# Kernel optimization log

Hardware: AMD Instinct MI355X
Metric: run time of the kernel (lower is better)

Reference implementation:

```python
import jax, jax.numpy as jnp
import numpy as np


def setup_inputs() -> dict:
    key = jax.random.key(0)
    k1, k2 = jax.random.split(key)
    B, H, W, C = 16, 4, 900, 256
    input_1 = jax.random.normal(k1, (B, H, W, C), dtype=jnp.float32)
    input_2 = jax.random.normal(k2, (B, H, W, C), dtype=jnp.float32)
    return {"input_1": input_1, "input_2": input_2}


def reference(input_1, input_2):
    # Original op: circularly pad input_1 along W (shift by n_pad), frame into W
    # overlapping windows of length W, multiply by input_2 and sum over (H, W, C).
    # Equivalent math: out[b, s] = sum_w <x1[b, :, (s + w + n_pad) % W, :],
    #                                     x2[b, :, w, :]>  (inner product over H, C).
    # We compute the [B, W, W] Gram matrix with a GEMM, then reduce the circular
    # diagonal bands -- avoids materializing the W-times framed [B, H, W, W, C].
    B, H, W, C = input_1.shape
    n_pad = W // 2
    D = H * C
    a1 = jnp.transpose(input_1, (0, 2, 1, 3)).reshape(B, W, D)  # [B, W, H*C]
    a2 = jnp.transpose(input_2, (0, 2, 1, 3)).reshape(B, W, D)
    gram = jnp.einsum('bid,bjd->bij', a1, a2)  # gram[b, i, j] = <x1_i, x2_j>
    s = jnp.arange(W)[:, None]   # shift index
    w = jnp.arange(W)[None, :]   # window position
    idx = (s + w + n_pad) % W    # [W, W] circular gather indices
    out = jnp.sum(gram[:, idx, w], axis=-1)  # [B, W]
    return out
```

## Files before the change

kernel.cpp:

```cpp
#include <hip/hip_runtime.h>
#include <stdint.h>

typedef __attribute__((ext_vector_type(8))) short short8;
typedef __attribute__((ext_vector_type(8))) unsigned short ushort8;
typedef __attribute__((ext_vector_type(4))) float floatx4;

#define W_DIM 900
#define PADW  1024
#define DDIM  1024
#define NPAD  450
#define TM    256
#define TN    128
#define BK    64

__device__ __forceinline__ unsigned short f2bf(float f) {
  unsigned int u = __builtin_bit_cast(unsigned int, f);
  u += 0x7fffu + ((u >> 16) & 1u);
  return (unsigned short)(u >> 16);
}

__device__ __forceinline__ void async16(const void* g, void* l) {
  __builtin_amdgcn_global_load_lds(
      (const __attribute__((address_space(1))) void*)g,
      (__attribute__((address_space(3))) void*)l, 16, 0, 0);
}

__global__ void convert_kernel(const float* __restrict__ in1,
                               const float* __restrict__ in2,
                               unsigned short* __restrict__ dA,
                               unsigned short* __restrict__ dB) {
  const int t  = threadIdx.x;
  const int w  = blockIdx.x * 2 + (t >> 7);
  const int b  = blockIdx.y;
  const float* __restrict__ src = blockIdx.z ? in2 : in1;
  unsigned short* __restrict__ dst = blockIdx.z ? dB : dA;

  const int tt = t & 127;
  const int h  = tt >> 5;
  const int c8 = (tt & 31) << 3;

  ushort8 o = (ushort8)0;
  if (w < W_DIM) {
    const size_t soff = (((size_t)(b * 4 + h) * W_DIM + w) * 256 + c8);
    float4 v0 = *reinterpret_cast<const float4*>(src + soff);
    float4 v1 = *reinterpret_cast<const float4*>(src + soff + 4);
    o[0] = f2bf(v0.x); o[1] = f2bf(v0.y); o[2] = f2bf(v0.z); o[3] = f2bf(v0.w);
    o[4] = f2bf(v1.x); o[5] = f2bf(v1.y); o[6] = f2bf(v1.z); o[7] = f2bf(v1.w);
  }
  const size_t doff = ((size_t)b * PADW + w) * DDIM + h * 256 + c8;
  *reinterpret_cast<ushort8*>(dst + doff) = o;
}

__global__ __launch_bounds__(256, 2)
void gemm_band_kernel(const unsigned short* __restrict__ A,
                      const unsigned short* __restrict__ B,
                      float* __restrict__ out) {
  const int b  = blockIdx.y;
  const int it = blockIdx.x >> 3;
  const int jt = blockIdx.x & 7;

  __shared__ __align__(16) unsigned char smem[49152];
  unsigned short* As = (unsigned short*)smem;
  unsigned short* Bs = (unsigned short*)smem + 16384;

  const int tid  = threadIdx.x;
  const int lane = tid & 63;
  const int warp = tid >> 6;
  const int wm   = warp >> 1;
  const int wn   = warp & 1;

  const unsigned short* Ab = A + ((size_t)(b * PADW + it * TM)) * DDIM;
  const unsigned short* Bb = B + ((size_t)(b * PADW + jt * TN)) * DDIM;

  const int r  = lane >> 2;
  const int ch = (lane & 3) << 3;

  const unsigned short* gA[8]; unsigned short* lA[8];
#pragma unroll
  for (int g = 0; g < 4; ++g)
#pragma unroll
    for (int s = 0; s < 2; ++s) {
      const int row = warp * 64 + g * 16 + r;
      gA[g * 2 + s] = Ab + (size_t)row * DDIM + s * 32 + ch;
      lA[g * 2 + s] = As + s * 8192 + row * 32 + ch;
    }
  const unsigned short* gB[4]; unsigned short* lB[4];
#pragma unroll
  for (int g = 0; g < 2; ++g)
#pragma unroll
    for (int s = 0; s < 2; ++s) {
      const int row = warp * 32 + g * 16 + r;
      gB[g * 2 + s] = Bb + (size_t)row * DDIM + s * 32 + ch;
      lB[g * 2 + s] = Bs + s * 4096 + row * 32 + ch;
    }

  floatx4 acc[8][4];
#pragma unroll
  for (int i = 0; i < 8; ++i)
#pragma unroll
    for (int j = 0; j < 4; ++j) acc[i][j] = (floatx4)0.0f;

  const int quad = lane >> 4;
  const int r16  = lane & 15;
  const unsigned short* ArowBase = As + (wm * 128 + r16) * 32 + quad * 8;
  const unsigned short* BrowBase = Bs + (wn * 64 + r16) * 32 + quad * 8;

  for (int kt = 0; kt < DDIM / BK; ++kt) {
    __syncthreads();
    const int ko = kt * BK;
#pragma unroll
    for (int i = 0; i < 8; ++i) async16(gA[i] + ko, lA[i]);
#pragma unroll
    for (int i = 0; i < 4; ++i) async16(gB[i] + ko, lB[i]);
    __syncthreads();

    for (int kc = 0; kc < 2; ++kc) {
      short8 af[8], bf[4];
#pragma unroll
      for (int mi = 0; mi < 8; ++mi)
        af[mi] = *(const short8*)(ArowBase + kc * 8192 + mi * 16 * 32);
#pragma unroll
      for (int ni = 0; ni < 4; ++ni)
        bf[ni] = *(const short8*)(BrowBase + kc * 4096 + ni * 16 * 32);
#pragma unroll
      for (int mi = 0; mi < 8; ++mi)
#pragma unroll
        for (int ni = 0; ni < 4; ++ni)
          acc[mi][ni] = __builtin_amdgcn_mfma_f32_16x16x32_bf16(
              af[mi], bf[ni], acc[mi][ni], 0, 0, 0);
    }
  }

  __syncthreads();
  float* Ep = (float*)smem;
  const int dbase = it * TM - jt * TN - NPAD;

  for (int p = 0; p < 4; ++p) {
    if (wm == (p >> 1)) {
      const int mib = (p & 1) * 4;
#pragma unroll
      for (int mo = 0; mo < 4; ++mo)
#pragma unroll
        for (int ni = 0; ni < 4; ++ni)
#pragma unroll
          for (int rr = 0; rr < 4; ++rr) {
            const int lr = mo * 16 + quad * 4 + rr;
            const int c  = wn * 64 + ni * 16 + r16;
            Ep[lr * 132 + c] = acc[mib + mo][ni][rr];
          }
    }
    __syncthreads();
    if (tid < 191) {
      const int d = tid - 127;
      int k0 = d > 0 ? d : 0;
      int k1 = 128 + d; if (k1 > 64) k1 = 64;
      float s = 0.0f;
      for (int k = k0; k < k1; ++k) s += Ep[k * 132 + (k - d)];
      int dg = dbase + p * 64 + d;
      int sidx = dg % W_DIM;
      if (sidx < 0) sidx += W_DIM;
      atomicAdd(&out[b * W_DIM + sidx], s);
    }
    __syncthreads();
  }
}

__global__ void naive_kernel(const float* __restrict__ x1,
                             const float* __restrict__ x2,
                             float* __restrict__ out) {
  const int s = blockIdx.x;
  const int b = blockIdx.y;
  const int c = threadIdx.x;
  float acc = 0.0f;
  for (int h = 0; h < 4; ++h) {
    const float* p1 = x1 + (size_t)(b * 4 + h) * W_DIM * 256;
    const float* p2 = x2 + (size_t)(b * 4 + h) * W_DIM * 256;
    for (int w = 0; w < W_DIM; ++w) {
      int w1 = s + w + NPAD;
      if (w1 >= W_DIM) w1 -= W_DIM;
      if (w1 >= W_DIM) w1 -= W_DIM;
      acc += p1[(size_t)w1 * 256 + c] * p2[(size_t)w * 256 + c];
    }
  }
  for (int off = 32; off > 0; off >>= 1) acc += __shfl_down(acc, off, 64);
  __shared__ float red[4];
  if ((threadIdx.x & 63) == 0) red[threadIdx.x >> 6] = acc;
  __syncthreads();
  if (threadIdx.x == 0)
    out[b * W_DIM + s] = red[0] + red[1] + red[2] + red[3];
}

extern "C" void kernel_launch(void* const* d_in, const int* in_sizes, int n_in,
                              void* d_out, int out_size, void* d_ws, size_t ws_size,
                              hipStream_t stream) {
  const float* x1 = (const float*)d_in[0];
  const float* x2 = (const float*)d_in[1];
  float* out = (float*)d_out;

  hipMemsetAsync(d_out, 0, (size_t)out_size * sizeof(float), stream);

  const size_t need = (size_t)2 * 16 * PADW * DDIM * sizeof(unsigned short);
  if (ws_size >= need) {
    unsigned short* dA = (unsigned short*)d_ws;
    unsigned short* dB = dA + (size_t)16 * PADW * DDIM;
    convert_kernel<<<dim3(512, 16, 2), 256, 0, stream>>>(x1, x2, dA, dB);
    gemm_band_kernel<<<dim3(32, 16), 256, 0, stream>>>(dA, dB, out);
  } else {
    naive_kernel<<<dim3(W_DIM, 16), 256, 0, stream>>>(x1, x2, out);
  }
}
```

Baseline: 193.0 us.

## Fuse fp32-to-bf16 conversion into gram GEMM and drop workspace staging

The separate conversion kernel and its bf16 workspace copy are removed. The GEMM now loads fp32 tiles straight from the inputs into registers, converts them to bf16, and stores them to padded LDS (stride 40). It prefetches the next K-slab into registers while the MFMAs run, and uses BK=32 with bounds masks in place of zero-padded rows. This saves the extra write and re-read of the bf16 copies, but the GEMM now re-reads fp32 data, which is twice the bytes and is fetched once per tile pair. Rounding also becomes round-half-up instead of round-to-nearest-even.

Measured after the change: 167.6 us. -13.1%, faster.

```diff
diff --git a/kernel.cpp b/kernel.cpp
--- a/kernel.cpp
+++ b/kernel.cpp
@@ -6,62 +6,28 @@
 typedef __attribute__((ext_vector_type(4))) float floatx4;
 
 #define W_DIM 900
-#define PADW  1024
-#define DDIM  1024
 #define NPAD  450
 #define TM    256
 #define TN    128
-#define BK    64
+#define BK    32
+#define LDST  40
 
 __device__ __forceinline__ unsigned short f2bf(float f) {
   unsigned int u = __builtin_bit_cast(unsigned int, f);
-  u += 0x7fffu + ((u >> 16) & 1u);
-  return (unsigned short)(u >> 16);
-}
-
-__device__ __forceinline__ void async16(const void* g, void* l) {
-  __builtin_amdgcn_global_load_lds(
-      (const __attribute__((address_space(1))) void*)g,
-      (__attribute__((address_space(3))) void*)l, 16, 0, 0);
-}
-
-__global__ void convert_kernel(const float* __restrict__ in1,
-                               const float* __restrict__ in2,
-                               unsigned short* __restrict__ dA,
-                               unsigned short* __restrict__ dB) {
-  const int t  = threadIdx.x;
-  const int w  = blockIdx.x * 2 + (t >> 7);
-  const int b  = blockIdx.y;
-  const float* __restrict__ src = blockIdx.z ? in2 : in1;
-  unsigned short* __restrict__ dst = blockIdx.z ? dB : dA;
-
-  const int tt = t & 127;
-  const int h  = tt >> 5;
-  const int c8 = (tt & 31) << 3;
-
-  ushort8 o = (ushort8)0;
-  if (w < W_DIM) {
-    const size_t soff = (((size_t)(b * 4 + h) * W_DIM + w) * 256 + c8);
-    float4 v0 = *reinterpret_cast<const float4*>(src + soff);
-    float4 v1 = *reinterpret_cast<const float4*>(src + soff + 4);
-    o[0] = f2bf(v0.x); o[1] = f2bf(v0.y); o[2] = f2bf(v0.z); o[3] = f2bf(v0.w);
-    o[4] = f2bf(v1.x); o[5] = f2bf(v1.y); o[6] = f2bf(v1.z); o[7] = f2bf(v1.w);
-  }
-  const size_t doff = ((size_t)b * PADW + w) * DDIM + h * 256 + c8;
-  *reinterpret_cast<ushort8*>(dst + doff) = o;
+  return (unsigned short)((u + 0x8000u) >> 16);
 }
 
 __global__ __launch_bounds__(256, 2)
-void gemm_band_kernel(const unsigned short* __restrict__ A,
-                      const unsigned short* __restrict__ B,
-                      float* __restrict__ out) {
-  const int b  = blockIdx.y;
-  const int it = blockIdx.x >> 3;
-  const int jt = blockIdx.x & 7;
+void fused_gram_band(const float* __restrict__ X1, const float* __restrict__ X2,
+                     float* __restrict__ out) {
+  const int x  = blockIdx.x;
+  const int b  = x & 15;
+  const int it = (x >> 4) & 3;
+  const int jt = x >> 6;
 
-  __shared__ __align__(16) unsigned char smem[49152];
+  __shared__ __align__(16) unsigned char smem[64 * 132 * 4];
   unsigned short* As = (unsigned short*)smem;
-  unsigned short* Bs = (unsigned short*)smem + 16384;
+  unsigned short* Bs = As + TM * LDST;
 
   const int tid  = threadIdx.x;
   const int lane = tid & 63;
@@ -69,30 +35,50 @@
   const int wm   = warp >> 1;
   const int wn   = warp & 1;
 
-  const unsigned short* Ab = A + ((size_t)(b * PADW + it * TM)) * DDIM;
-  const unsigned short* Bb = B + ((size_t)(b * PADW + jt * TN)) * DDIM;
+  const int rsub = lane >> 2;
+  const int c8   = (lane & 3) << 3;
 
-  const int r  = lane >> 2;
-  const int ch = (lane & 3) << 3;
+  int arow[4], brow[2];
+  bool aok[4], bok[2];
+#pragma unroll
+  for (int s = 0; s < 4; ++s) {
+    arow[s] = it * TM + warp * 64 + s * 16 + rsub;
+    aok[s]  = arow[s] < W_DIM;
+  }
+#pragma unroll
+  for (int s = 0; s < 2; ++s) {
+    brow[s] = jt * TN + warp * 32 + s * 16 + rsub;
+    bok[s]  = brow[s] < W_DIM;
+  }
 
-  const unsigned short* gA[8]; unsigned short* lA[8];
-#pragma unroll
-  for (int g = 0; g < 4; ++g)
-#pragma unroll
-    for (int s = 0; s < 2; ++s) {
-      const int row = warp * 64 + g * 16 + r;
-      gA[g * 2 + s] = Ab + (size_t)row * DDIM + s * 32 + ch;
-      lA[g * 2 + s] = As + s * 8192 + row * 32 + ch;
-    }
-  const unsigned short* gB[4]; unsigned short* lB[4];
-#pragma unroll
-  for (int g = 0; g < 2; ++g)
-#pragma unroll
-    for (int s = 0; s < 2; ++s) {
-      const int row = warp * 32 + g * 16 + r;
-      gB[g * 2 + s] = Bb + (size_t)row * DDIM + s * 32 + ch;
-      lB[g * 2 + s] = Bs + s * 4096 + row * 32 + ch;
-    }
+  const size_t bbase = (size_t)b * 4 * W_DIM * 256;
+
+  float4 va[4][2], vb[2][2];
+  const float4 fz = make_float4(0.f, 0.f, 0.f, 0.f);
+
+#define LOAD_SLAB(kt)                                                          \
+  {                                                                            \
+    const size_t koff = bbase + (size_t)((kt) >> 3) * (W_DIM * 256) +          \
+                        ((kt) & 7) * 32 + c8;                                  \
+    _Pragma("unroll")                                                          \
+    for (int s = 0; s < 4; ++s) {                                              \
+      va[s][0] = fz; va[s][1] = fz;                                            \
+      if (aok[s]) {                                                            \
+        const float* p = X1 + koff + (size_t)arow[s] * 256;                    \
+        va[s][0] = *(const float4*)p;                                          \
+        va[s][1] = *(const float4*)(p + 4);                                    \
+      }                                                                        \
+    }                                                                          \
+    _Pragma("unroll")                                                          \
+    for (int s = 0; s < 2; ++s) {                                              \
+      vb[s][0] = fz; vb[s][1] = fz;                                            \
+      if (bok[s]) {                                                            \
+        const float* p = X2 + koff + (size_t)brow[s] * 256;                    \
+        vb[s][0] = *(const float4*)p;                                          \
+        vb[s][1] = *(const float4*)(p + 4);                                    \
+      }                                                                        \
+    }                                                                          \
+  }
 
   floatx4 acc[8][4];
 #pragma unroll
@@ -102,33 +88,48 @@
 
   const int quad = lane >> 4;
   const int r16  = lane & 15;
-  const unsigned short* ArowBase = As + (wm * 128 + r16) * 32 + quad * 8;
-  const unsigned short* BrowBase = Bs + (wn * 64 + r16) * 32 + quad * 8;
+  const unsigned short* ArowBase = As + (wm * 128 + r16) * LDST + quad * 8;
+  const unsigned short* BrowBase = Bs + (wn * 64 + r16) * LDST + quad * 8;
 
-  for (int kt = 0; kt < DDIM / BK; ++kt) {
+  LOAD_SLAB(0);
+
+  for (int kt = 0; kt < 32; ++kt) {
     __syncthreads();
-    const int ko = kt * BK;
 #pragma unroll
-    for (int i = 0; i < 8; ++i) async16(gA[i] + ko, lA[i]);
+    for (int s = 0; s < 4; ++s) {
+      ushort8 o;
+      o[0] = f2bf(va[s][0].x); o[1] = f2bf(va[s][0].y);
+      o[2] = f2bf(va[s][0].z); o[3] = f2bf(va[s][0].w);
+      o[4] = f2bf(va[s][1].x); o[5] = f2bf(va[s][1].y);
+      o[6] = f2bf(va[s][1].z); o[7] = f2bf(va[s][1].w);
+      *(ushort8*)&As[(warp * 64 + s * 16 + rsub) * LDST + c8] = o;
+    }
 #pragma unroll
-    for (int i = 0; i < 4; ++i) async16(gB[i] + ko, lB[i]);
+    for (int s = 0; s < 2; ++s) {
+      ushort8 o;
+      o[0] = f2bf(vb[s][0].x); o[1] = f2bf(vb[s][0].y);
+      o[2] = f2bf(vb[s][0].z); o[3] = f2bf(vb[s][0].w);
+      o[4] = f2bf(vb[s][1].x); o[5] = f2bf(vb[s][1].y);
+      o[6] = f2bf(vb[s][1].z); o[7] = f2bf(vb[s][1].w);
+      *(ushort8*)&Bs[(warp * 32 + s * 16 + rsub) * LDST + c8] = o;
+    }
     __syncthreads();
 
-    for (int kc = 0; kc < 2; ++kc) {
-      short8 af[8], bf[4];
+    if (kt < 31) LOAD_SLAB(kt + 1);
+
+    short8 af[8], bf[4];
 #pragma unroll
-      for (int mi = 0; mi < 8; ++mi)
-        af[mi] = *(const short8*)(ArowBase + kc * 8192 + mi * 16 * 32);
+    for (int mi = 0; mi < 8; ++mi)
+      af[mi] = *(const short8*)(ArowBase + mi * 16 * LDST);
+#pragma unroll
+    for (int ni = 0; ni < 4; ++ni)
+      bf[ni] = *(const short8*)(BrowBase + ni * 16 * LDST);
+#pragma unroll
+    for (int mi = 0; mi < 8; ++mi)
 #pragma unroll
       for (int ni = 0; ni < 4; ++ni)
-        bf[ni] = *(const short8*)(BrowBase + kc * 4096 + ni * 16 * 32);
-#pragma unroll
-      for (int mi = 0; mi < 8; ++mi)
-#pragma unroll
-        for (int ni = 0; ni < 4; ++ni)
-          acc[mi][ni] = __builtin_amdgcn_mfma_f32_16x16x32_bf16(
-              af[mi], bf[ni], acc[mi][ni], 0, 0, 0);
-    }
+        acc[mi][ni] = __builtin_amdgcn_mfma_f32_16x16x32_bf16(
+            af[mi], bf[ni], acc[mi][ni], 0, 0, 0);
   }
 
   __syncthreads();
@@ -165,31 +166,6 @@
   }
 }
 
-__global__ void naive_kernel(const float* __restrict__ x1,
-                             const float* __restrict__ x2,
-                             float* __restrict__ out) {
-  const int s = blockIdx.x;
-  const int b = blockIdx.y;
-  const int c = threadIdx.x;
-  float acc = 0.0f;
-  for (int h = 0; h < 4; ++h) {
-    const float* p1 = x1 + (size_t)(b * 4 + h) * W_DIM * 256;
-    const float* p2 = x2 + (size_t)(b * 4 + h) * W_DIM * 256;
-    for (int w = 0; w < W_DIM; ++w) {
-      int w1 = s + w + NPAD;
-      if (w1 >= W_DIM) w1 -= W_DIM;
-      if (w1 >= W_DIM) w1 -= W_DIM;
-      acc += p1[(size_t)w1 * 256 + c] * p2[(size_t)w * 256 + c];
-    }
-  }
-  for (int off = 32; off > 0; off >>= 1) acc += __shfl_down(acc, off, 64);
-  __shared__ float red[4];
-  if ((threadIdx.x & 63) == 0) red[threadIdx.x >> 6] = acc;
-  __syncthreads();
-  if (threadIdx.x == 0)
-    out[b * W_DIM + s] = red[0] + red[1] + red[2] + red[3];
-}
-
 extern "C" void kernel_launch(void* const* d_in, const int* in_sizes, int n_in,
                               void* d_out, int out_size, void* d_ws, size_t ws_size,
                               hipStream_t stream) {
@@ -198,14 +174,5 @@
   float* out = (float*)d_out;
 
   hipMemsetAsync(d_out, 0, (size_t)out_size * sizeof(float), stream);
-
-  const size_t need = (size_t)2 * 16 * PADW * DDIM * sizeof(unsigned short);
-  if (ws_size >= need) {
-    unsigned short* dA = (unsigned short*)d_ws;
-    unsigned short* dB = dA + (size_t)16 * PADW * DDIM;
-    convert_kernel<<<dim3(512, 16, 2), 256, 0, stream>>>(x1, x2, dA, dB);
-    gemm_band_kernel<<<dim3(32, 16), 256, 0, stream>>>(dA, dB, out);
-  } else {
-    naive_kernel<<<dim3(W_DIM, 16), 256, 0, stream>>>(x1, x2, out);
-  }
+  fused_gram_band<<<dim3(512), 256, 0, stream>>>(x1, x2, out);
 }
```

## Store bf16 operands in K-slab layout with XOR swizzle and batch-interleaved grid

Applied to the files above, without the earlier changes.

The convert kernel now transposes data through shared memory into a slab layout: each batch is split into 32-column K slabs, and within a slab rows are contiguous and XOR-swizzled. The GEMM can then load each tile with fully contiguous per-lane async loads and read LDS with fewer bank conflicts. The GEMM grid is flattened so that consecutive blocks belong to different batches, and the bf16 rounding is simplified to round-half-up. These changes target global-load coalescing and LDS conflicts. The cost is an extra shared-memory pass in the convert kernel and a slightly different rounding rule.

Measured after the change: 187.1 us. 3.0% less time.

```diff
diff --git a/kernel.cpp b/kernel.cpp
--- a/kernel.cpp
+++ b/kernel.cpp
@@ -6,17 +6,15 @@
 typedef __attribute__((ext_vector_type(4))) float floatx4;
 
 #define W_DIM 900
-#define PADW  1024
-#define DDIM  1024
 #define NPAD  450
 #define TM    256
 #define TN    128
-#define BK    64
+#define SLAB_E   32768
+#define BATCH_E  1048576
 
 __device__ __forceinline__ unsigned short f2bf(float f) {
   unsigned int u = __builtin_bit_cast(unsigned int, f);
-  u += 0x7fffu + ((u >> 16) & 1u);
-  return (unsigned short)(u >> 16);
+  return (unsigned short)((u + 0x8000u) >> 16);
 }
 
 __device__ __forceinline__ void async16(const void* g, void* l) {
@@ -25,43 +23,63 @@
       (__attribute__((address_space(3))) void*)l, 16, 0, 0);
 }
 
-__global__ void convert_kernel(const float* __restrict__ in1,
-                               const float* __restrict__ in2,
+__global__ void convert_kernel(const float* __restrict__ X1,
+                               const float* __restrict__ X2,
                                unsigned short* __restrict__ dA,
                                unsigned short* __restrict__ dB) {
+  const int wt = blockIdx.x;
+  const int h  = blockIdx.y;
+  const int bz = blockIdx.z;
+  const int b  = bz & 15;
+  const float* __restrict__ src = (bz >> 4) ? X2 : X1;
+  unsigned short* __restrict__ dst = (bz >> 4) ? dB : dA;
+
+  __shared__ __align__(16) unsigned short T[64 * 264];
+
   const int t  = threadIdx.x;
-  const int w  = blockIdx.x * 2 + (t >> 7);
-  const int b  = blockIdx.y;
-  const float* __restrict__ src = blockIdx.z ? in2 : in1;
-  unsigned short* __restrict__ dst = blockIdx.z ? dB : dA;
-
-  const int tt = t & 127;
-  const int h  = tt >> 5;
-  const int c8 = (tt & 31) << 3;
-
-  ushort8 o = (ushort8)0;
-  if (w < W_DIM) {
-    const size_t soff = (((size_t)(b * 4 + h) * W_DIM + w) * 256 + c8);
-    float4 v0 = *reinterpret_cast<const float4*>(src + soff);
-    float4 v1 = *reinterpret_cast<const float4*>(src + soff + 4);
-    o[0] = f2bf(v0.x); o[1] = f2bf(v0.y); o[2] = f2bf(v0.z); o[3] = f2bf(v0.w);
-    o[4] = f2bf(v1.x); o[5] = f2bf(v1.y); o[6] = f2bf(v1.z); o[7] = f2bf(v1.w);
-  }
-  const size_t doff = ((size_t)b * PADW + w) * DDIM + h * 256 + c8;
-  *reinterpret_cast<ushort8*>(dst + doff) = o;
+  const int c8 = (t & 31) << 3;
+#pragma unroll
+  for (int i = 0; i < 8; ++i) {
+    const int wl = i * 8 + (t >> 5);
+    const int wg = wt * 64 + wl;
+    ushort8 o = (ushort8)0;
+    if (wg < W_DIM) {
+      const float* p = src + (((size_t)(b * 4 + h) * W_DIM + wg) << 8) + c8;
+      float4 v0 = *(const float4*)p;
+      float4 v1 = *(const float4*)(p + 4);
+      o[0] = f2bf(v0.x); o[1] = f2bf(v0.y); o[2] = f2bf(v0.z); o[3] = f2bf(v0.w);
+      o[4] = f2bf(v1.x); o[5] = f2bf(v1.y); o[6] = f2bf(v1.z); o[7] = f2bf(v1.w);
+    }
+    *(ushort8*)&T[wl * 264 + c8] = o;
+  }
+  __syncthreads();
+
+  const int wl = t >> 2;
+  const int wg = wt * 64 + wl;
+  const int ch = t & 3;
+  const int c0 = ch ^ (wl & 3);
+#pragma unroll
+  for (int s = 0; s < 8; ++s) {
+    ushort8 v = *(const ushort8*)&T[wl * 264 + s * 32 + c0 * 8];
+    const size_t off =
+        ((size_t)b * BATCH_E) + (size_t)(h * 8 + s) * SLAB_E + (size_t)wg * 32 + ch * 8;
+    *(ushort8*)&dst[off] = v;
+  }
 }
 
 __global__ __launch_bounds__(256, 2)
 void gemm_band_kernel(const unsigned short* __restrict__ A,
                       const unsigned short* __restrict__ B,
                       float* __restrict__ out) {
-  const int b  = blockIdx.y;
-  const int it = blockIdx.x >> 3;
-  const int jt = blockIdx.x & 7;
+  const int x    = blockIdx.x;
+  const int b    = x & 15;
+  const int pair = x >> 4;
+  const int it   = pair >> 3;
+  const int jt   = pair & 7;
 
   __shared__ __align__(16) unsigned char smem[49152];
   unsigned short* As = (unsigned short*)smem;
-  unsigned short* Bs = (unsigned short*)smem + 16384;
+  unsigned short* Bs = As + 16384;
 
   const int tid  = threadIdx.x;
   const int lane = tid & 63;
@@ -69,30 +87,12 @@
   const int wm   = warp >> 1;
   const int wn   = warp & 1;
 
-  const unsigned short* Ab = A + ((size_t)(b * PADW + it * TM)) * DDIM;
-  const unsigned short* Bb = B + ((size_t)(b * PADW + jt * TN)) * DDIM;
-
-  const int r  = lane >> 2;
-  const int ch = (lane & 3) << 3;
-
-  const unsigned short* gA[8]; unsigned short* lA[8];
-#pragma unroll
-  for (int g = 0; g < 4; ++g)
-#pragma unroll
-    for (int s = 0; s < 2; ++s) {
-      const int row = warp * 64 + g * 16 + r;
-      gA[g * 2 + s] = Ab + (size_t)row * DDIM + s * 32 + ch;
-      lA[g * 2 + s] = As + s * 8192 + row * 32 + ch;
-    }
-  const unsigned short* gB[4]; unsigned short* lB[4];
-#pragma unroll
-  for (int g = 0; g < 2; ++g)
-#pragma unroll
-    for (int s = 0; s < 2; ++s) {
-      const int row = warp * 32 + g * 16 + r;
-      gB[g * 2 + s] = Bb + (size_t)row * DDIM + s * 32 + ch;
-      lB[g * 2 + s] = Bs + s * 4096 + row * 32 + ch;
-    }
+  const unsigned short* gAlane =
+      A + (size_t)b * BATCH_E + (size_t)(it * TM + warp * 64) * 32 + lane * 8;
+  const unsigned short* gBlane =
+      B + (size_t)b * BATCH_E + (size_t)(jt * TN + warp * 32) * 32 + lane * 8;
+  unsigned short* lA = As + warp * 64 * 32 + lane * 8;
+  unsigned short* lB = Bs + warp * 32 * 32 + lane * 8;
 
   floatx4 acc[8][4];
 #pragma unroll
@@ -102,26 +102,33 @@
 
   const int quad = lane >> 4;
   const int r16  = lane & 15;
-  const unsigned short* ArowBase = As + (wm * 128 + r16) * 32 + quad * 8;
-  const unsigned short* BrowBase = Bs + (wn * 64 + r16) * 32 + quad * 8;
-
-  for (int kt = 0; kt < DDIM / BK; ++kt) {
-    __syncthreads();
-    const int ko = kt * BK;
-#pragma unroll
-    for (int i = 0; i < 8; ++i) async16(gA[i] + ko, lA[i]);
-#pragma unroll
-    for (int i = 0; i < 4; ++i) async16(gB[i] + ko, lB[i]);
-    __syncthreads();
-
-    for (int kc = 0; kc < 2; ++kc) {
+  const int csw  = (quad ^ (r16 & 3)) * 8;
+  const unsigned short* ArowBase = As + (wm * 128 + r16) * 32 + csw;
+  const unsigned short* BrowBase = Bs + (wn * 64 + r16) * 32 + csw;
+
+  for (int kt = 0; kt < 16; ++kt) {
+    __syncthreads();
+    const size_t ko = (size_t)kt * (2 * SLAB_E);
+#pragma unroll
+    for (int s = 0; s < 2; ++s) {
+#pragma unroll
+      for (int g = 0; g < 4; ++g)
+        async16(gAlane + ko + s * SLAB_E + g * 512, lA + s * 8192 + g * 512);
+#pragma unroll
+      for (int g = 0; g < 2; ++g)
+        async16(gBlane + ko + s * SLAB_E + g * 512, lB + s * 4096 + g * 512);
+    }
+    __syncthreads();
+
+#pragma unroll
+    for (int s = 0; s < 2; ++s) {
       short8 af[8], bf[4];
 #pragma unroll
       for (int mi = 0; mi < 8; ++mi)
-        af[mi] = *(const short8*)(ArowBase + kc * 8192 + mi * 16 * 32);
+        af[mi] = *(const short8*)(ArowBase + s * 8192 + mi * 512);
 #pragma unroll
       for (int ni = 0; ni < 4; ++ni)
-        bf[ni] = *(const short8*)(BrowBase + kc * 4096 + ni * 16 * 32);
+        bf[ni] = *(const short8*)(BrowBase + s * 4096 + ni * 512);
 #pragma unroll
       for (int mi = 0; mi < 8; ++mi)
 #pragma unroll
@@ -199,12 +206,12 @@
 
   hipMemsetAsync(d_out, 0, (size_t)out_size * sizeof(float), stream);
 
-  const size_t need = (size_t)2 * 16 * PADW * DDIM * sizeof(unsigned short);
+  const size_t need = (size_t)2 * 16 * BATCH_E * sizeof(unsigned short);
   if (ws_size >= need) {
     unsigned short* dA = (unsigned short*)d_ws;
-    unsigned short* dB = dA + (size_t)16 * PADW * DDIM;
-    convert_kernel<<<dim3(512, 16, 2), 256, 0, stream>>>(x1, x2, dA, dB);
-    gemm_band_kernel<<<dim3(32, 16), 256, 0, stream>>>(dA, dB, out);
+    unsigned short* dB = dA + (size_t)16 * BATCH_E;
+    convert_kernel<<<dim3(16, 4, 32), 256, 0, stream>>>(x1, x2, dA, dB);
+    gemm_band_kernel<<<dim3(512), 256, 0, stream>>>(dA, dB, out);
   } else {
     naive_kernel<<<dim3(W_DIM, 16), 256, 0, stream>>>(x1, x2, out);
   }
```
